# Kernel optimization log

Measured on AMD Instinct MI355X. Metric: run time of the kernel, lower is better.

Reference implementation:

```python
import jax, jax.numpy as jnp
import numpy as np

NU = 0.01
RHO = 1.0
WSCALE = 0.05  # keep activations sane for deep randn-initialized MLP


def _mlp(z, Win, b_in, Wh, b_h, Wout, b_out):
    # z: (3,) -> (2,) = (psi, p)
    h = jax.nn.relu(z @ Win + b_in)
    for i in range(Wh.shape[0]):  # static, small layer loop
        h = jax.nn.relu(h @ Wh[i] + b_h[i])
    return h @ Wout + b_out


def _point(z, Win, b_in, Wh, b_h, Wout, b_out):
    # z = (x, y, t)
    psi_fn = lambda zz: _mlp(zz, Win, b_in, Wh, b_h, Wout, b_out)[0]
    p_fn = lambda zz: _mlp(zz, Win, b_in, Wh, b_h, Wout, b_out)[1]
    u_fn = lambda zz: jax.grad(psi_fn)(zz)[1]   # u = dpsi/dy
    v_fn = lambda zz: -jax.grad(psi_fn)(zz)[0]  # v = -dpsi/dx
    u = u_fn(z)
    v = v_fn(z)
    p = p_fn(z)
    gu = jax.grad(u_fn)(z)   # (u_x, u_y, u_t)
    gv = jax.grad(v_fn)(z)   # (v_x, v_y, v_t)
    gp = jax.grad(p_fn)(z)   # (p_x, p_y, p_t)
    Hu = jax.jacfwd(jax.grad(u_fn))(z)  # 3x3 Hessian of u
    Hv = jax.jacfwd(jax.grad(v_fn))(z)
    f = gu[2] + u * gu[0] + v * gu[1] + gp[0] / RHO - NU * (Hu[0, 0] + Hu[1, 1])
    g = gv[2] + u * gv[0] + v * gv[1] + gp[1] / RHO - NU * (Hv[0, 0] + Hv[1, 1])
    return u, v, p, f, g


def setup_inputs() -> dict:
    key = jax.random.key(0)
    ks = jax.random.split(key, 6)
    N, H, L = 65536, 256, 6
    x = jax.random.normal(ks[0], (N, 1), dtype=jnp.float32)
    y = jax.random.normal(ks[1], (N, 1), dtype=jnp.float32)
    t = jax.random.uniform(ks[2], (N, 1), dtype=jnp.float32)
    Win = jax.random.normal(ks[3], (3, H), dtype=jnp.float32) * WSCALE
    b_in = jnp.zeros((H,), dtype=jnp.float32)
    Wh = jax.random.normal(ks[4], (L - 2, H, H), dtype=jnp.float32) * WSCALE
    b_h = jnp.zeros((L - 2, H), dtype=jnp.float32)
    Wout = jax.random.normal(ks[5], (H, 2), dtype=jnp.float32) * WSCALE
    b_out = jnp.zeros((2,), dtype=jnp.float32)
    return {"x": x, "y": y, "t": t, "Win": Win, "b_in": b_in,
            "Wh": Wh, "b_h": b_h, "Wout": Wout, "b_out": b_out}


def reference(x, y, t, Win, b_in, Wh, b_h, Wout, b_out):
    z = jnp.concatenate([x, y, t], axis=1)  # (N, 3)
    u, v, p, f, g = jax.vmap(_point, in_axes=(0, None, None, None, None, None, None))(
        z, Win, b_in, Wh, b_h, Wout, b_out)
    col = lambda a: a[:, None]  # (N,) -> (N,1)
    return col(u), col(v), col(p), col(f), col(g)
```

## Files before the change

### kernel.cpp

```cpp
#include <hip/hip_runtime.h>
#include <hip/hip_bf16.h>


#define NPTS 65536
#define HDIM 256

typedef _Float16 half8_t __attribute__((ext_vector_type(8)));
typedef _Float16 half4_t __attribute__((ext_vector_type(4)));
typedef float floatx4 __attribute__((ext_vector_type(4)));

__global__ void __launch_bounds__(512) fwd_fused_kernel(
    const float* __restrict__ x, const float* __restrict__ y, const float* __restrict__ t,
    const float* __restrict__ Win, const float* __restrict__ b_in,
    const float* __restrict__ Wh, const float* __restrict__ b_h,
    const float* __restrict__ Wout, const float* __restrict__ b_out,
    unsigned char* __restrict__ masks, float* __restrict__ out) {
  constexpr int SH = 257;
  __shared__ float hT[64 * SH];
  __shared__ float pscr[8][72];

  const int tid = threadIdx.x;
  const int lane = tid & 63;
  const int w = __builtin_amdgcn_readfirstlane(tid >> 6);
  const int c0 = w * 32;
  const int p0 = blockIdx.x * 64;
  const int p = p0 + lane;

  {
    float xv = x[p], yv = y[p], tv = t[p];
    unsigned m = 0;
#pragma unroll
    for (int e = 0; e < 32; ++e) {
      int c = c0 + e;
      float dot = fmaf(xv, Win[c], 0.f);
      dot = fmaf(yv, Win[256 + c], dot);
      dot = fmaf(tv, Win[512 + c], dot);
      float a = dot + b_in[c];
      bool pos = a > 0.f;
      hT[lane * SH + c] = pos ? a : 0.f;
      m |= (pos ? 1u : 0u) << e;
    }
    *(unsigned*)(masks + (size_t)p * 32 + w * 4) = m;
  }
  __syncthreads();

  for (int l = 0; l < 4; ++l) {
    const float* Wl = Wh + (size_t)l * 65536 + c0;
    float acc[32] = {};
#pragma unroll 2
    for (int k = 0; k < 256; ++k) {
      float h = hT[lane * SH + k];
      const float* wr = Wl + k * 256;
#pragma unroll
      for (int e = 0; e < 32; ++e)
        acc[e] = fmaf(h, wr[e], acc[e]);
    }
    __syncthreads();
    unsigned m = 0;
    float hnew[32];
#pragma unroll
    for (int e = 0; e < 32; ++e) {
      float a = acc[e] + b_h[l * 256 + c0 + e];
      bool pos = a > 0.f;
      hnew[e] = pos ? a : 0.f;
      m |= (pos ? 1u : 0u) << e;
    }
    *(unsigned*)(masks + ((size_t)(l + 1) * NPTS + p) * 32 + w * 4) = m;
#pragma unroll
    for (int e = 0; e < 32; ++e)
      hT[lane * SH + c0 + e] = hnew[e];
    __syncthreads();
  }

  float s = 0.f;
#pragma unroll
  for (int e = 0; e < 32; ++e)
    s = fmaf(hT[lane * SH + c0 + e], Wout[2 * (c0 + e) + 1], s);
  pscr[w][lane] = s;
  __syncthreads();
  if (tid < 64) {
    float s2 = 0.f;
#pragma unroll
    for (int g = 0; g < 8; ++g) s2 += pscr[g][tid];
    out[2 * NPTS + p0 + tid] = s2 + b_out[1];
  }
}

__global__ void __launch_bounds__(256) prep_weights_kernel(
    const float* __restrict__ Wh, _Float16* __restrict__ Wt) {
  int i = blockIdx.x * 256 + threadIdx.x;
  int l = i >> 16;
  int rem = i & 65535;
  int k = rem >> 8, n = rem & 255;
  Wt[(size_t)(l << 16) + n * 256 + k] = (_Float16)Wh[i];
}

__global__ void __launch_bounds__(256, 2) tangent_fused_kernel(
    const float* __restrict__ Win,
    const _Float16* __restrict__ Wt,
    const unsigned int* __restrict__ maskDw,
    const float* __restrict__ Wout, float* __restrict__ out) {
  constexpr int SA = 264;
  constexpr int SB = 72;
  __shared__ alignas(16) _Float16 Apan[64 * SA];
  __shared__ alignas(16) _Float16 Bpan[256 * SB];
  __shared__ unsigned int smask[5 * 256];

  const int tid = threadIdx.x;
  const int lane = tid & 63;
  const int wn = tid >> 6;
  const int l15 = lane & 15, quad = lane >> 4;
  const int p0 = blockIdx.x * 32;

#pragma unroll
  for (int i = 0; i < 5; ++i)
    smask[i * 256 + tid] = maskDw[(size_t)i * NPTS * 8 + (size_t)p0 * 8 + tid];
  __syncthreads();

#pragma unroll
  for (int i = 0; i < 8; ++i) {
    int g = tid + 256 * i;
    int row = g >> 5, cg = g & 31;
    int c0 = cg * 8, pt = row & 31, tg = row >> 5;
    unsigned dw = smask[pt * 8 + (c0 >> 5)];
    half8_t v;
#pragma unroll
    for (int e = 0; e < 8; ++e) {
      bool m = (dw >> ((cg & 3) * 8 + e)) & 1;
      v[e] = m ? (_Float16)Win[tg * 256 + c0 + e] : (_Float16)0.f;
    }
    *(half8_t*)&Apan[row * SA + c0] = v;
  }

  for (int l = 0; l < 4; ++l) {
    const _Float16* Wl = Wt + (size_t)l * 65536;
    floatx4 acc[4][4] = {};
    for (int kp = 0; kp < 4; ++kp) {
      __syncthreads();
#pragma unroll
      for (int i = 0; i < 8; ++i) {
        int g = tid + 256 * i;
        int row = g >> 3, seg = g & 7;
        *(half8_t*)&Bpan[row * SB + seg * 8] =
            *(const half8_t*)(Wl + (size_t)row * 256 + kp * 64 + seg * 8);
      }
      __syncthreads();
#pragma unroll
      for (int ks = 0; ks < 2; ++ks) {
        half8_t af[4], bf[4];
#pragma unroll
        for (int mi = 0; mi < 4; ++mi)
          af[mi] = *(const half8_t*)&Apan[(mi * 16 + l15) * SA + kp * 64 + ks * 32 + quad * 8];
#pragma unroll
        for (int nj = 0; nj < 4; ++nj)
          bf[nj] = *(const half8_t*)&Bpan[(wn * 64 + nj * 16 + l15) * SB + ks * 32 + quad * 8];
#pragma unroll
        for (int mi = 0; mi < 4; ++mi)
#pragma unroll
          for (int nj = 0; nj < 4; ++nj)
            acc[mi][nj] = __builtin_amdgcn_mfma_f32_16x16x32_f16(af[mi], bf[nj], acc[mi][nj], 0, 0, 0);
      }
    }
    __syncthreads();
    const unsigned int* ml = &smask[(l + 1) * 256];
#pragma unroll
    for (int mi = 0; mi < 4; ++mi) {
#pragma unroll
      for (int r = 0; r < 4; ++r) {
        int row = mi * 16 + quad * 4 + r;
        int pt = row & 31;
#pragma unroll
        for (int nj = 0; nj < 4; ++nj) {
          int C = wn * 64 + nj * 16 + l15;
          bool m = (ml[pt * 8 + (C >> 5)] >> (C & 31)) & 1;
          Apan[row * SA + C] = m ? (_Float16)acc[mi][nj][r] : (_Float16)0.f;
        }
      }
    }
    __syncthreads();
  }

  float4 wA = *(const float4*)(Wout + lane * 8);
  float4 wB = *(const float4*)(Wout + lane * 8 + 4);
  float w0[4] = {wA.x, wA.z, wB.x, wB.z};
  float w1[4] = {wA.y, wA.w, wB.y, wB.w};
#pragma unroll
  for (int i = 0; i < 16; ++i) {
    int row = wn * 16 + i;
    half4_t hv = *(const half4_t*)&Apan[row * SA + lane * 4];
    float s0 = 0.f, s1 = 0.f;
#pragma unroll
    for (int e = 0; e < 4; ++e) {
      float fv = (float)hv[e];
      s0 = fmaf(fv, w0[e], s0);
      s1 = fmaf(fv, w1[e], s1);
    }
#pragma unroll
    for (int off = 1; off < 64; off <<= 1) {
      s0 += __shfl_xor(s0, off);
      s1 += __shfl_xor(s1, off);
    }
    if (lane == 0) {
      int pt = p0 + (row & 31);
      if (row < 32) {
        out[NPTS + pt] = -s0;
        out[3 * NPTS + pt] = s1;
      } else {
        out[pt] = s0;
        out[4 * NPTS + pt] = s1;
      }
    }
  }
}

extern "C" void kernel_launch(void* const* d_in, const int* in_sizes, int n_in,
                              void* d_out, int out_size, void* d_ws, size_t ws_size,
                              hipStream_t stream) {
  const float* x = (const float*)d_in[0];
  const float* y = (const float*)d_in[1];
  const float* t = (const float*)d_in[2];
  const float* Win = (const float*)d_in[3];
  const float* b_in = (const float*)d_in[4];
  const float* Wh = (const float*)d_in[5];
  const float* b_h = (const float*)d_in[6];
  const float* Wout = (const float*)d_in[7];
  const float* b_out = (const float*)d_in[8];
  float* out = (float*)d_out;

  char* ws = (char*)d_ws;
  constexpr size_t MASK_SZ = (size_t)NPTS * 32;
  unsigned char* masks = (unsigned char*)ws;
  _Float16* Wt = (_Float16*)(ws + 5 * MASK_SZ);

  prep_weights_kernel<<<1024, 256, 0, stream>>>(Wh, Wt);

  fwd_fused_kernel<<<NPTS / 64, 512, 0, stream>>>(
      x, y, t, Win, b_in, Wh, b_h, Wout, b_out, masks, out);

  tangent_fused_kernel<<<NPTS / 32, 256, 0, stream>>>(
      Win, Wt, (const unsigned int*)masks, Wout, out);
}
```

Baseline: 599.1 us.

## Move forward-pass activations from LDS to global ping-pong buffers

The forward kernel stops keeping the 64x256 activation tile in shared memory. Activations now go to two global buffers laid out feature-major, swapped between layers, and the last layer's values stay in registers for the output dot product. This frees about 66 KB of LDS per block so more blocks can be resident, at the cost of 64 MB of extra global traffic per layer and a dependence on L2/MALL caching for the reads.

```diff
diff --git a/kernel.cpp b/kernel.cpp
--- a/kernel.cpp
+++ b/kernel.cpp
@@ -14,9 +14,8 @@
     const float* __restrict__ Win, const float* __restrict__ b_in,
     const float* __restrict__ Wh, const float* __restrict__ b_h,
     const float* __restrict__ Wout, const float* __restrict__ b_out,
+    float* __restrict__ bufA, float* __restrict__ bufB,
     unsigned char* __restrict__ masks, float* __restrict__ out) {
-  constexpr int SH = 257;
-  __shared__ float hT[64 * SH];
   __shared__ float pscr[8][72];
 
   const int tid = threadIdx.x;
@@ -37,45 +36,50 @@
       dot = fmaf(tv, Win[512 + c], dot);
       float a = dot + b_in[c];
       bool pos = a > 0.f;
-      hT[lane * SH + c] = pos ? a : 0.f;
+      bufA[(size_t)c * NPTS + p] = pos ? a : 0.f;
       m |= (pos ? 1u : 0u) << e;
     }
     *(unsigned*)(masks + (size_t)p * 32 + w * 4) = m;
   }
   __syncthreads();
 
+  float* bin = bufA;
+  float* bout = bufB;
+  float hlast[32];
   for (int l = 0; l < 4; ++l) {
     const float* Wl = Wh + (size_t)l * 65536 + c0;
+    const float* hp = bin + p;
     float acc[32] = {};
 #pragma unroll 2
     for (int k = 0; k < 256; ++k) {
-      float h = hT[lane * SH + k];
+      float h = hp[(size_t)k * NPTS];
       const float* wr = Wl + k * 256;
 #pragma unroll
       for (int e = 0; e < 32; ++e)
         acc[e] = fmaf(h, wr[e], acc[e]);
     }
-    __syncthreads();
     unsigned m = 0;
-    float hnew[32];
 #pragma unroll
     for (int e = 0; e < 32; ++e) {
       float a = acc[e] + b_h[l * 256 + c0 + e];
       bool pos = a > 0.f;
-      hnew[e] = pos ? a : 0.f;
+      hlast[e] = pos ? a : 0.f;
       m |= (pos ? 1u : 0u) << e;
     }
     *(unsigned*)(masks + ((size_t)(l + 1) * NPTS + p) * 32 + w * 4) = m;
-#pragma unroll
-    for (int e = 0; e < 32; ++e)
-      hT[lane * SH + c0 + e] = hnew[e];
-    __syncthreads();
+    if (l < 3) {
+#pragma unroll
+      for (int e = 0; e < 32; ++e)
+        bout[(size_t)(c0 + e) * NPTS + p] = hlast[e];
+      __syncthreads();
+      float* tmp = bin; bin = bout; bout = tmp;
+    }
   }
 
   float s = 0.f;
 #pragma unroll
   for (int e = 0; e < 32; ++e)
-    s = fmaf(hT[lane * SH + c0 + e], Wout[2 * (c0 + e) + 1], s);
+    s = fmaf(hlast[e], Wout[2 * (c0 + e) + 1], s);
   pscr[w][lane] = s;
   __syncthreads();
   if (tid < 64) {
@@ -228,14 +232,17 @@
   float* out = (float*)d_out;
 
   char* ws = (char*)d_ws;
+  constexpr size_t BUF_SZ = (size_t)NPTS * 256 * 4;
   constexpr size_t MASK_SZ = (size_t)NPTS * 32;
-  unsigned char* masks = (unsigned char*)ws;
-  _Float16* Wt = (_Float16*)(ws + 5 * MASK_SZ);
+  float* bufA = (float*)ws;
+  float* bufB = (float*)(ws + BUF_SZ);
+  unsigned char* masks = (unsigned char*)(ws + 2 * BUF_SZ);
+  _Float16* Wt = (_Float16*)(ws + 2 * BUF_SZ + 5 * MASK_SZ);
 
   prep_weights_kernel<<<1024, 256, 0, stream>>>(Wh, Wt);
 
   fwd_fused_kernel<<<NPTS / 64, 512, 0, stream>>>(
-      x, y, t, Win, b_in, Wh, b_h, Wout, b_out, masks, out);
+      x, y, t, Win, b_in, Wh, b_h, Wout, b_out, bufA, bufB, masks, out);
 
   tangent_fused_kernel<<<NPTS / 32, 256, 0, stream>>>(
       Win, Wt, (const unsigned int*)masks, Wout, out);
```

Result: slower. 825.9 us (+37.8%).
